# Kernel optimization log

Measured on AMD Instinct MI355X. Metric: run time of the kernel, lower is better.

Reference implementation:

```python
import jax, jax.numpy as jnp
import numpy as np

N_T = 200
THR = 0.6
ALPHA = 0.8   # hard-coded in __init__
KAPPA = 0.8   # hard-coded in __init__
RHO = 0.97
BETA = 0.07
SCALE = 50.0  # get_pos scale
# norse defaults used by ConstantCurrentLIFEncoder / LILinearCell
DT = 1e-3
TAU_MEM_INV = 100.0
TAU_SYN_INV = 200.0
V_TH = 1.0


def encode_constant_current(I):
    """norse ConstantCurrentLIFEncoder: LIF driven by constant current I [n_b, f] -> spikes [n_t, n_b, f]."""
    def step(v, _):
        v = v + DT * TAU_MEM_INV * (I - v)          # dv = dt*tau_mem_inv*((v_leak - v) + I), v_leak=0
        z = (v > V_TH).astype(I.dtype)
        v = v * (1.0 - z)                            # reset to v_reset=0 on spike
        return v, z
    _, zs = jax.lax.scan(step, jnp.zeros_like(I), None, length=N_T)
    return zs


def setup_inputs() -> dict:
    key = jax.random.key(0)
    ks = jax.random.split(key, 5)
    n_b, n_feat = 128, 512
    n_in, n_rec, n_out = 2 * n_feat, 2048, 32
    x = jax.random.normal(ks[0], (n_b, n_feat), jnp.float32)
    # kaiming_normal_ std = sqrt(2/fan_in), then scaled by w_init_gain
    w_in = jax.random.normal(ks[1], (n_rec, n_in), jnp.float32) * (0.5 * np.sqrt(2.0 / n_in))
    w_rec = jax.random.normal(ks[2], (n_rec, n_rec), jnp.float32) * (0.1 * np.sqrt(2.0 / n_rec))
    w_out = jax.random.normal(ks[3], (n_out, n_rec), jnp.float32) * (0.5 * np.sqrt(2.0 / n_rec))
    w_li = jax.random.normal(ks[4], (1, n_rec), jnp.float32) * np.sqrt(2.0 / n_rec)
    return {"x": x, "w_in": w_in, "w_rec": w_rec, "w_out": w_out, "w_li": w_li}


def reference(x, w_in, w_rec, w_out, w_li):
    n_rec = w_rec.shape[0]
    n_out = w_out.shape[0]
    n_b = x.shape[0]
    # get_pos: pos/neg rectified constant-current LIF encoding, cat on feature dim -> [n_t, n_b, n_in]
    xs = jnp.concatenate([
        encode_constant_current(jax.nn.relu(SCALE * x)),
        encode_constant_current(jax.nn.relu(-SCALE * x)),
    ], axis=2)
    # zero self-recurrence: w_rec *= (1 - I)
    w_rec = w_rec * (1.0 - jnp.eye(n_rec, dtype=w_rec.dtype))

    def step(carry, x_t):
        v, a, z, vo, li_v, li_i = carry
        # ALIF membrane update + adaptive threshold spike
        v = ALPHA * v + z @ w_rec.T + x_t @ w_in.T - z * THR
        a = RHO * a + z
        z = (v > THR + BETA * a).astype(v.dtype)
        # (dropout p=0.5 treated as identity / eval mode)
        vo = KAPPA * vo + z @ w_out.T
        # norse LILinearCell critic readout (li_step)
        i_jump = li_i + z @ w_li.T
        li_v = li_v + DT * TAU_MEM_INV * (i_jump - li_v)
        li_i = i_jump - DT * TAU_SYN_INV * i_jump
        return (v, a, z, vo, li_v, li_i), (vo, li_v)

    zeros = lambda d: jnp.zeros((n_b, d), x.dtype)
    carry0 = (zeros(n_rec), zeros(n_rec), zeros(n_rec), zeros(n_out), zeros(1), zeros(1))
    _, (vo_seq, vc_seq) = jax.lax.scan(step, carry0, xs[: N_T - 1])  # loop runs n_t-1 steps
    # torch.max over time includes the all-zero t=0 row -> clamp max with 0
    m = jnp.maximum(jnp.max(vo_seq, axis=0), 0.0)          # [n_b, n_out]
    yo = jax.nn.softmax(m, axis=1)
    critic_value = jnp.maximum(jnp.max(vc_seq, axis=0), 0.0)  # [n_b, 1]
    return yo, critic_value
```

## Files before the change

### kernel.cpp

```cpp
#include <hip/hip_runtime.h>
#include <cstdint>
#include <cstddef>

typedef __attribute__((ext_vector_type(8))) short short8;
typedef __attribute__((ext_vector_type(4))) float f32x4;
typedef __attribute__((ext_vector_type(4))) unsigned int u32x4;

union U4S8 { u32x4 u; short8 s; unsigned w[4]; };

#define TSTEPS 199

#define WF_PLANE 786432u
#define WR_BASE  1572864u
#define WR_PLANE 12288u

#define WS_BAR  0u
#define WS_ZB   4096u
#define WS_FIN  135168u
#define WS_XSB  151552u
#define WS_WF   3411968u
#define WS_NEED 28971008u

#define AT_RLX __ATOMIC_RELAXED
#define SC_AGT __HIP_MEMORY_SCOPE_AGENT

extern "C" __global__ __launch_bounds__(1024) void k_encode(
    const float* __restrict__ x, unsigned char* __restrict__ xsb)
{
  const int b = blockIdx.x;
  const int tid = threadIdx.x;
  const float xv = (tid < 512) ? x[b * 512 + tid] : x[b * 512 + tid - 512];
  const float I = (tid < 512) ? fmaxf(__fmul_rn(50.0f, xv), 0.0f)
                              : fmaxf(__fmul_rn(-50.0f, xv), 0.0f);
  float v = 0.0f;
  unsigned long long* dst =
      (unsigned long long*)(xsb + (size_t)b * 128u + (size_t)(tid >> 6) * 8u);
  for (int t = 0; t < TSTEPS; ++t) {
    v = __fadd_rn(v, __fmul_rn(0.1f, __fsub_rn(I, v)));
    const bool z = v > 1.0f;
    if (z) v = 0.0f;
    const unsigned long long m = __ballot(z ? 1 : 0);
    if ((tid & 63) == 0) dst[(size_t)t * 2048u] = m;
  }
}

__device__ __forceinline__ unsigned bf16rne(float f) {
  const unsigned u = __float_as_uint(f);
  return ((u + 0x7FFFu + ((u >> 16) & 1u)) >> 16) & 0xFFFFu;
}

extern "C" __global__ __launch_bounds__(256) void k_prep(
    const float* __restrict__ w_rec, const float* __restrict__ w_in,
    const float* __restrict__ w_out, const float* __restrict__ w_li,
    u32x4* __restrict__ wf)
{
  const unsigned idx  = blockIdx.x * 256u + threadIdx.x;
  const unsigned lane = idx & 63u;
  if (idx < 786432u) {
    const unsigned kt = (idx >> 6) % 96u;
    const unsigned ns = idx / 6144u;
    const unsigned j  = ns * 16u + (lane & 15u);
    const unsigned k0 = kt * 32u + (lane >> 4) * 8u;
    unsigned hi[4], lo[4];
#pragma unroll
    for (int u2 = 0; u2 < 4; ++u2) {
      unsigned hb[2], lb[2];
#pragma unroll
      for (int c = 0; c < 2; ++c) {
        const unsigned k = k0 + 2u * (unsigned)u2 + (unsigned)c;
        float w;
        if (k < 2048u) w = (k == j) ? 0.0f : w_rec[(size_t)j * 2048u + k];
        else           w = w_in[(size_t)j * 1024u + (k - 2048u)];
        const unsigned h = bf16rne(w);
        const float hvf = __uint_as_float(h << 16);
        const unsigned l = bf16rne(__fsub_rn(w, hvf));
        hb[c] = h; lb[c] = l;
      }
      hi[u2] = hb[0] | (hb[1] << 16);
      lo[u2] = lb[0] | (lb[1] << 16);
    }
    u32x4 vh, vl;
    vh[0]=hi[0]; vh[1]=hi[1]; vh[2]=hi[2]; vh[3]=hi[3];
    vl[0]=lo[0]; vl[1]=lo[1]; vl[2]=lo[2]; vl[3]=lo[3];
    wf[idx] = vh;
    wf[idx + WF_PLANE] = vl;
  } else if (idx < 786432u + 12288u) {
    const unsigned r   = idx - 786432u;
    const unsigned kt  = (r >> 6) & 63u;
    const unsigned nsr = r >> 12;
    const unsigned o   = nsr * 16u + (lane & 15u);
    const unsigned k0  = kt * 32u + (lane >> 4) * 8u;
    unsigned hi[4], lo[4];
#pragma unroll
    for (int u2 = 0; u2 < 4; ++u2) {
      unsigned hb[2], lb[2];
#pragma unroll
      for (int c = 0; c < 2; ++c) {
        const unsigned k = k0 + 2u * (unsigned)u2 + (unsigned)c;
        float w = 0.0f;
        if (o < 32u)       w = w_out[(size_t)o * 2048u + k];
        else if (o == 32u) w = w_li[k];
        const unsigned h = bf16rne(w);
        const float hvf = __uint_as_float(h << 16);
        hb[c] = h;
        lb[c] = bf16rne(__fsub_rn(w, hvf));
      }
      hi[u2] = hb[0] | (hb[1] << 16);
      lo[u2] = lb[0] | (lb[1] << 16);
    }
    u32x4 vh, vl;
    vh[0]=hi[0]; vh[1]=hi[1]; vh[2]=hi[2]; vh[3]=hi[3];
    vl[0]=lo[0]; vl[1]=lo[1]; vl[2]=lo[2]; vl[3]=lo[3];
    wf[WR_BASE + r] = vh;
    wf[WR_BASE + WR_PLANE + r] = vl;
  }
}

__device__ __forceinline__ void bar_arrive(unsigned* dbar, unsigned ns)
{
  __syncthreads();
  if (threadIdx.x == 0) {
    __hip_atomic_fetch_add(dbar + (ns >> 4) * 16u, 1u, AT_RLX, SC_AGT);
  }
}

__device__ __forceinline__ void bar_wait16(unsigned* dbar, unsigned tgt16)
{
  if (threadIdx.x == 0) {
    for (;;) {
      unsigned mn = 0xFFFFFFFFu;
#pragma unroll
      for (int g = 0; g < 8; ++g) {
        const unsigned c = __hip_atomic_load(dbar + g * 16, AT_RLX, SC_AGT);
        mn = (c < mn) ? c : mn;
      }
      if (mn >= tgt16) break;
      __builtin_amdgcn_s_sleep(2);
    }
    asm volatile("" ::: "memory");
  }
  __syncthreads();
}

extern "C" __global__ __launch_bounds__(512) void k_main(
    const u32x4* __restrict__ wf,
    const unsigned char* __restrict__ xsb,
    unsigned* __restrict__ zb,
    unsigned* __restrict__ bar,
    unsigned* __restrict__ fin,
    float* __restrict__ out)
{
  __shared__ unsigned abytes[64][100];
  __shared__ float red[8][64][17];
  __shared__ unsigned char zn[64][4];
  __shared__ float pad_lds[6000];

  const unsigned tid  = threadIdx.x;
  const unsigned wg   = blockIdx.x;
  const unsigned mh   = wg >> 7;
  const unsigned ns   = wg & 127u;
  const unsigned wv   = tid >> 6;
  const unsigned lane = tid & 63u;
  const unsigned ln15 = lane & 15u;
  const unsigned g4   = lane >> 4;
  const unsigned selr = g4 * 0x01010101u;
  const unsigned blq  = tid & 63u;
  const unsigned q    = tid >> 6;
  const bool     upd  = tid < 256u;
  const bool     dual = ns < 3u;

  if (tid == 0) ((volatile float*)pad_lds)[0] = 0.f;

  unsigned* dbar = bar + mh * 256u;

  const u32x4* WH = wf + (size_t)ns * 6144u;
  const u32x4* WL = wf + WF_PLANE + (size_t)ns * 6144u;
  const u32x4* RH = wf + WR_BASE + (size_t)ns * 4096u;
  const u32x4* RL = wf + WR_BASE + WR_PLANE + (size_t)ns * 4096u;

  float v[4]  = {0,0,0,0}, a[4] = {0,0,0,0}, zf[4] = {0,0,0,0};
  float vo[4] = {0,0,0,0}, voMax[4] = {0,0,0,0};
  float liv = 0.f, lii = 0.f, liMax = 0.f;

  f32x4 accX0 = {0,0,0,0}, accX1 = {0,0,0,0}, accX2 = {0,0,0,0}, accX3 = {0,0,0,0};
  U4S8 bhZ[8], blZ[8];
  const int zk = (int)wv * 8;
  const int xk = 64 + (int)wv * 4;

  auto pk = [](unsigned long long t) -> unsigned {
    return (unsigned)(t & 0xFFFFu) | (unsigned)(((t >> 32) & 0xFFFFu) << 16);
  };

  auto stage_xs = [&](int t) {
    const unsigned char* xr = xsb + ((size_t)t * 128u + mh * 64u) * 128u;
    const u32x4 val = *(const u32x4*)(xr + (size_t)lane * 128u + wv * 16u);
    *(u32x4*)&abytes[lane][64u + wv * 4u] = val;
  };

  auto mk = [&](unsigned dw, U4S8& af) {
    const unsigned sp = __builtin_amdgcn_perm(dw, dw, selr);
    const unsigned W  = ((sp >> 1) & 0xFFFF0000u) | (sp & 0x0000FFFFu);
    af.w[0] = __umul24(W & 0x00010001u, 0x3F80u);
    af.w[1] = __umul24(W & 0x00040004u, 0x0FE0u);
    af.w[2] = __umul24(W & 0x00100010u, 0x03F8u);
    af.w[3] = __umul24(W & 0x00400040u, 0x00FEu);
  };

  auto dosub2 = [&](unsigned dw, const short8& bhj, const short8& blj, f32x4& ACC) {
    U4S8 af; mk(dw, af);
    ACC = __builtin_amdgcn_mfma_f32_16x16x32_bf16(af.s, bhj, ACC, 0, 0, 0);
    ACC = __builtin_amdgcn_mfma_f32_16x16x32_bf16(af.s, blj, ACC, 0, 0, 0);
  };

  auto ldw = [&](const u32x4* H, const u32x4* L, int kb, U4S8* bh, U4S8* bl) {
#pragma unroll
    for (int j = 0; j < 4; ++j) {
      bh[j].u = H[(size_t)(kb + j) * 64u + lane];
      bl[j].u = L[(size_t)(kb + j) * 64u + lane];
    }
  };

  auto grp4 = [&](int kb, const U4S8* bh, const U4S8* bl) {
    U4S8 a0, a1, a2, a3;
    a0.u = *(const u32x4*)&abytes[ 0 + ln15][kb];
    a1.u = *(const u32x4*)&abytes[16 + ln15][kb];
    a2.u = *(const u32x4*)&abytes[32 + ln15][kb];
    a3.u = *(const u32x4*)&abytes[48 + ln15][kb];
#pragma unroll
    for (int j = 0; j < 4; ++j) {
      dosub2(a0.w[j], bh[j].s, bl[j].s, accX0);
      dosub2(a1.w[j], bh[j].s, bl[j].s, accX1);
      dosub2(a2.w[j], bh[j].s, bl[j].s, accX2);
      dosub2(a3.w[j], bh[j].s, bl[j].s, accX3);
    }
  };

  auto compute_accX = [&]() {
    U4S8 bh2[4], bl2[4];
    accX0 = {0,0,0,0}; accX1 = {0,0,0,0}; accX2 = {0,0,0,0}; accX3 = {0,0,0,0};
    ldw(WH, WL, xk, bh2, bl2);
    grp4(xk, bh2, bl2);
  };

  auto prefetchZ = [&]() {
#pragma unroll
    for (int j = 0; j < 8; ++j) {
      bhZ[j].u = WH[(size_t)(zk + j) * 64u + lane];
      blZ[j].u = WL[(size_t)(zk + j) * 64u + lane];
    }
  };

  auto stage_and_zpart = [&](unsigned buf) {
    const unsigned long long* zp = (const unsigned long long*)zb +
        ((size_t)((buf * 2u + mh) * 64u + lane) * 64u) + (unsigned)zk;
    unsigned long long z0 = __hip_atomic_load(zp + 0, AT_RLX, SC_AGT);
    unsigned long long z1 = __hip_atomic_load(zp + 1, AT_RLX, SC_AGT);
    unsigned long long z2 = __hip_atomic_load(zp + 2, AT_RLX, SC_AGT);
    unsigned long long z3 = __hip_atomic_load(zp + 3, AT_RLX, SC_AGT);
    unsigned long long z4 = __hip_atomic_load(zp + 4, AT_RLX, SC_AGT);
    unsigned long long z5 = __hip_atomic_load(zp + 5, AT_RLX, SC_AGT);
    unsigned long long z6 = __hip_atomic_load(zp + 6, AT_RLX, SC_AGT);
    unsigned long long z7 = __hip_atomic_load(zp + 7, AT_RLX, SC_AGT);
    u32x4 wa; wa[0] = pk(z0); wa[1] = pk(z1); wa[2] = pk(z2); wa[3] = pk(z3);
    *(u32x4*)&abytes[lane][(unsigned)zk] = wa;
    grp4(zk, &bhZ[0], &blZ[0]);
    u32x4 wb; wb[0] = pk(z4); wb[1] = pk(z5); wb[2] = pk(z6); wb[3] = pk(z7);
    *(u32x4*)&abytes[lane][(unsigned)zk + 4u] = wb;
    grp4(zk + 4, &bhZ[4], &blZ[4]);
  };

  auto redstore = [&]() {
#pragma unroll
    for (int r = 0; r < 4; ++r) {
      red[wv][ 0 + g4 * 4 + r][ln15] = accX0[r];
      red[wv][16 + g4 * 4 + r][ln15] = accX1[r];
      red[wv][32 + g4 * 4 + r][ln15] = accX2[r];
      red[wv][48 + g4 * 4 + r][ln15] = accX3[r];
    }
  };

  auto readout_pass = [&]() {
    f32x4 r0 = {0,0,0,0}, r1 = {0,0,0,0}, r2 = {0,0,0,0}, r3 = {0,0,0,0};
    const int kb = (int)wv * 8;
#pragma unroll
    for (int kc = 0; kc < 8; kc += 4) {
      U4S8 ar0, ar1, ar2, ar3;
      ar0.u = *(const u32x4*)&abytes[ 0 + ln15][kb + kc];
      ar1.u = *(const u32x4*)&abytes[16 + ln15][kb + kc];
      ar2.u = *(const u32x4*)&abytes[32 + ln15][kb + kc];
      ar3.u = *(const u32x4*)&abytes[48 + ln15][kb + kc];
      U4S8 bh[4], bl[4];
#pragma unroll
      for (int j = 0; j < 4; ++j) {
        bh[j].u = RH[(size_t)(kb + kc + j) * 64u + lane];
        bl[j].u = RL[(size_t)(kb + kc + j) * 64u + lane];
      }
#pragma unroll
      for (int j = 0; j < 4; ++j) {
        U4S8 af0; mk(ar0.w[j], af0);
        r0 = __builtin_amdgcn_mfma_f32_16x16x32_bf16(af0.s, bh[j].s, r0, 0, 0, 0);
        r0 = __builtin_amdgcn_mfma_f32_16x16x32_bf16(af0.s, bl[j].s, r0, 0, 0, 0);
        U4S8 af1; mk(ar1.w[j], af1);
        r1 = __builtin_amdgcn_mfma_f32_16x16x32_bf16(af1.s, bh[j].s, r1, 0, 0, 0);
        r1 = __builtin_amdgcn_mfma_f32_16x16x32_bf16(af1.s, bl[j].s, r1, 0, 0, 0);
        U4S8 af2; mk(ar2.w[j], af2);
        r2 = __builtin_amdgcn_mfma_f32_16x16x32_bf16(af2.s, bh[j].s, r2, 0, 0, 0);
        r2 = __builtin_amdgcn_mfma_f32_16x16x32_bf16(af2.s, bl[j].s, r2, 0, 0, 0);
        U4S8 af3; mk(ar3.w[j], af3);
        r3 = __builtin_amdgcn_mfma_f32_16x16x32_bf16(af3.s, bh[j].s, r3, 0, 0, 0);
        r3 = __builtin_amdgcn_mfma_f32_16x16x32_bf16(af3.s, bl[j].s, r3, 0, 0, 0);
      }
    }
#pragma unroll
    for (int r = 0; r < 4; ++r) {
      red[wv][ 0 + g4 * 4 + r][ln15] = r0[r];
      red[wv][16 + g4 * 4 + r][ln15] = r1[r];
      red[wv][32 + g4 * 4 + r][ln15] = r2[r];
      red[wv][48 + g4 * 4 + r][ln15] = r3[r];
    }
    __syncthreads();
    if (upd) {
      if (ns < 2u) {
#pragma unroll
        for (int jj = 0; jj < 4; ++jj) {
          const unsigned n = q * 4u + (unsigned)jj;
          float s = ((red[0][blq][n] + red[1][blq][n]) + (red[2][blq][n] + red[3][blq][n]))
                  + ((red[4][blq][n] + red[5][blq][n]) + (red[6][blq][n] + red[7][blq][n]));
          vo[jj] = __fadd_rn(__fmul_rn(0.8f, vo[jj]), s);
          voMax[jj] = fmaxf(voMax[jj], vo[jj]);
        }
      } else if (q == 0u) {
        float s = ((red[0][blq][0] + red[1][blq][0]) + (red[2][blq][0] + red[3][blq][0]))
                + ((red[4][blq][0] + red[5][blq][0]) + (red[6][blq][0] + red[7][blq][0]));
        const float ij = __fadd_rn(lii, s);
        liv = __fadd_rn(liv, __fmul_rn(0.1f, __fsub_rn(ij, liv)));
        lii = __fsub_rn(ij, __fmul_rn(0.2f, ij));
        liMax = fmaxf(liMax, liv);
      }
    }
    __syncthreads();
  };

  stage_xs(0);
  compute_accX();
  prefetchZ();

  for (int t = 0; t < TSTEPS; ++t) {
    if (t > 0) bar_wait16(dbar, 16u * (unsigned)t);

    stage_and_zpart((unsigned)t & 1u);
    redstore();
    __syncthreads();

    if (upd) {
      unsigned nib = 0u;
#pragma unroll
      for (int jj = 0; jj < 4; ++jj) {
        const unsigned n = q * 4u + (unsigned)jj;
        const float dv = ((red[0][blq][n] + red[1][blq][n]) + (red[2][blq][n] + red[3][blq][n]))
                       + ((red[4][blq][n] + red[5][blq][n]) + (red[6][blq][n] + red[7][blq][n]));
        const float vv = __fsub_rn(__fadd_rn(__fmul_rn(0.8f, v[jj]), dv),
                                   __fmul_rn(zf[jj], 0.6f));
        a[jj] = __fadd_rn(__fmul_rn(0.97f, a[jj]), zf[jj]);
        const float th = __fadd_rn(0.6f, __fmul_rn(0.07f, a[jj]));
        const bool znew = vv > th;
        zf[jj] = znew ? 1.0f : 0.0f;
        v[jj] = vv;
        nib |= (znew ? 1u : 0u) << jj;
      }
      zn[blq][q] = (unsigned char)nib;
    }
    __syncthreads();

    if (tid < 64u) {
      const unsigned m16 = (unsigned)zn[tid][0] | ((unsigned)zn[tid][1] << 4) |
                           ((unsigned)zn[tid][2] << 8) | ((unsigned)zn[tid][3] << 12);
      const unsigned nb = ((unsigned)t & 1u) ^ 1u;
      __hip_atomic_store(zb + ((nb * 2u + mh) * 64u + tid) * 128u + ns, m16,
                         AT_RLX, SC_AGT);
    }
    bar_arrive(dbar, ns);

    if (t < TSTEPS - 1) stage_xs(t + 1);
    if (dual && t > 0) readout_pass();
    if (t < TSTEPS - 1) {
      compute_accX();
      prefetchZ();
    }
  }

  bar_wait16(dbar, 16u * (unsigned)TSTEPS);
  if (dual) {
    const unsigned buf = (unsigned)TSTEPS & 1u;
    const unsigned long long* zp = (const unsigned long long*)zb +
        ((size_t)((buf * 2u + mh) * 64u + lane) * 64u) + (unsigned)zk;
    u32x4 wa, wb;
    wa[0] = pk(__hip_atomic_load(zp + 0, AT_RLX, SC_AGT));
    wa[1] = pk(__hip_atomic_load(zp + 1, AT_RLX, SC_AGT));
    wa[2] = pk(__hip_atomic_load(zp + 2, AT_RLX, SC_AGT));
    wa[3] = pk(__hip_atomic_load(zp + 3, AT_RLX, SC_AGT));
    wb[0] = pk(__hip_atomic_load(zp + 4, AT_RLX, SC_AGT));
    wb[1] = pk(__hip_atomic_load(zp + 5, AT_RLX, SC_AGT));
    wb[2] = pk(__hip_atomic_load(zp + 6, AT_RLX, SC_AGT));
    wb[3] = pk(__hip_atomic_load(zp + 7, AT_RLX, SC_AGT));
    *(u32x4*)&abytes[lane][(unsigned)zk] = wa;
    *(u32x4*)&abytes[lane][(unsigned)zk + 4u] = wb;
    readout_pass();
    if (ns < 2u && upd) {
#pragma unroll
      for (int jj = 0; jj < 4; ++jj) {
        __hip_atomic_store(fin + ((size_t)mh * 64u + blq) * 32u + ns * 16u + q * 4u + (unsigned)jj,
                           __float_as_uint(voMax[jj]), AT_RLX, SC_AGT);
      }
    }
    if (ns == 2u && tid < 64u) {
      out[4096u + mh * 64u + tid] = liMax;
    }
  }
  bar_arrive(dbar, ns);

  if (ns == 0u) {
    bar_wait16(dbar, 16u * ((unsigned)TSTEPS + 1u));
    if (tid < 64u) {
      const unsigned grow = mh * 64u + tid;
      float vals[32];
#pragma unroll
      for (int o = 0; o < 32; ++o)
        vals[o] = __uint_as_float(__hip_atomic_load(fin + (size_t)grow * 32u + o,
                                                    AT_RLX, SC_AGT));
      float mx = vals[0];
#pragma unroll
      for (int o = 1; o < 32; ++o) mx = fmaxf(mx, vals[o]);
      float ssum = 0.f;
#pragma unroll
      for (int o = 0; o < 32; ++o) ssum += expf(vals[o] - mx);
      const float inv = 1.0f / ssum;
#pragma unroll
      for (int o = 0; o < 32; ++o) out[(size_t)grow * 32u + o] = expf(vals[o] - mx) * inv;
    }
  }
}

extern "C" void kernel_launch(void* const* d_in, const int* in_sizes, int n_in,
                              void* d_out, int out_size, void* d_ws, size_t ws_size,
                              hipStream_t stream)
{
  (void)in_sizes; (void)n_in; (void)out_size;
  if (ws_size < (size_t)WS_NEED) return;

  const float* x     = (const float*)d_in[0];
  const float* w_in  = (const float*)d_in[1];
  const float* w_rec = (const float*)d_in[2];
  const float* w_out = (const float*)d_in[3];
  const float* w_li  = (const float*)d_in[4];
  unsigned char* ws  = (unsigned char*)d_ws;

  unsigned*      bar  = (unsigned*)(ws + WS_BAR);
  unsigned*      zb   = (unsigned*)(ws + WS_ZB);
  unsigned*      fin  = (unsigned*)(ws + WS_FIN);
  unsigned char* xsb  = ws + WS_XSB;
  u32x4*         wf   = (u32x4*)(ws + WS_WF);

  hipMemsetAsync(bar, 0, 4096, stream);
  hipMemsetAsync(zb, 0, 131072, stream);
  k_encode<<<dim3(128), dim3(1024), 0, stream>>>(x, xsb);
  k_prep<<<dim3(3120), dim3(256), 0, stream>>>(w_rec, w_in, w_out, w_li, wf);
  k_main<<<dim3(256), dim3(512), 0, stream>>>(wf, xsb, zb, bar, fin, (float*)d_out);
}
```

Baseline: 1.793 ms.

## Replace grid barrier with tagged spike ring buffer and keep weights in registers

```diff
diff --git a/kernel.cpp b/kernel.cpp
--- a/kernel.cpp
+++ b/kernel.cpp
@@ -14,12 +14,12 @@
 #define WR_BASE  1572864u
 #define WR_PLANE 12288u
 
-#define WS_BAR  0u
-#define WS_ZB   4096u
-#define WS_FIN  135168u
-#define WS_XSB  151552u
-#define WS_WF   3411968u
-#define WS_NEED 28971008u
+#define WS_BAR    0u
+#define WS_ZROLL  4096u
+#define WS_FIN    528384u
+#define WS_XSB    544768u
+#define WS_WF     3805184u
+#define WS_NEED   29364224u
 
 #define AT_RLX __ATOMIC_RELAXED
 #define SC_AGT __HIP_MEMORY_SCOPE_AGENT
@@ -116,36 +116,10 @@
   }
 }
 
-__device__ __forceinline__ void bar_arrive(unsigned* dbar, unsigned ns)
-{
-  __syncthreads();
-  if (threadIdx.x == 0) {
-    __hip_atomic_fetch_add(dbar + (ns >> 4) * 16u, 1u, AT_RLX, SC_AGT);
-  }
-}
-
-__device__ __forceinline__ void bar_wait16(unsigned* dbar, unsigned tgt16)
-{
-  if (threadIdx.x == 0) {
-    for (;;) {
-      unsigned mn = 0xFFFFFFFFu;
-#pragma unroll
-      for (int g = 0; g < 8; ++g) {
-        const unsigned c = __hip_atomic_load(dbar + g * 16, AT_RLX, SC_AGT);
-        mn = (c < mn) ? c : mn;
-      }
-      if (mn >= tgt16) break;
-      __builtin_amdgcn_s_sleep(2);
-    }
-    asm volatile("" ::: "memory");
-  }
-  __syncthreads();
-}
-
-extern "C" __global__ __launch_bounds__(512) void k_main(
+extern "C" __global__ __launch_bounds__(512, 2) void k_main(
     const u32x4* __restrict__ wf,
     const unsigned char* __restrict__ xsb,
-    unsigned* __restrict__ zb,
+    unsigned* __restrict__ zroll,
     unsigned* __restrict__ bar,
     unsigned* __restrict__ fin,
     float* __restrict__ out)
@@ -171,8 +145,6 @@
 
   if (tid == 0) ((volatile float*)pad_lds)[0] = 0.f;
 
-  unsigned* dbar = bar + mh * 256u;
-
   const u32x4* WH = wf + (size_t)ns * 6144u;
   const u32x4* WL = wf + WF_PLANE + (size_t)ns * 6144u;
   const u32x4* RH = wf + WR_BASE + (size_t)ns * 4096u;
@@ -184,17 +156,16 @@
 
   f32x4 accX0 = {0,0,0,0}, accX1 = {0,0,0,0}, accX2 = {0,0,0,0}, accX3 = {0,0,0,0};
   U4S8 bhZ[8], blZ[8];
+  U4S8 bhX[4], blX[4];
   const int zk = (int)wv * 8;
   const int xk = 64 + (int)wv * 4;
 
   auto pk = [](unsigned long long t) -> unsigned {
     return (unsigned)(t & 0xFFFFu) | (unsigned)(((t >> 32) & 0xFFFFu) << 16);
   };
-
-  auto stage_xs = [&](int t) {
-    const unsigned char* xr = xsb + ((size_t)t * 128u + mh * 64u) * 128u;
-    const u32x4 val = *(const u32x4*)(xr + (size_t)lane * 128u + wv * 16u);
-    *(u32x4*)&abytes[lane][64u + wv * 4u] = val;
+  auto tagok = [](unsigned long long z, unsigned tg) -> bool {
+    return (((unsigned)(z >> 16) & 0xFFFFu) == tg) &&
+           (((unsigned)(z >> 48) & 0xFFFFu) == tg);
   };
 
   auto mk = [&](unsigned dw, U4S8& af) {
@@ -212,14 +183,6 @@
     ACC = __builtin_amdgcn_mfma_f32_16x16x32_bf16(af.s, blj, ACC, 0, 0, 0);
   };
 
-  auto ldw = [&](const u32x4* H, const u32x4* L, int kb, U4S8* bh, U4S8* bl) {
-#pragma unroll
-    for (int j = 0; j < 4; ++j) {
-      bh[j].u = H[(size_t)(kb + j) * 64u + lane];
-      bl[j].u = L[(size_t)(kb + j) * 64u + lane];
-    }
-  };
-
   auto grp4 = [&](int kb, const U4S8* bh, const U4S8* bl) {
     U4S8 a0, a1, a2, a3;
     a0.u = *(const u32x4*)&abytes[ 0 + ln15][kb];
@@ -236,35 +199,37 @@
   };
 
   auto compute_accX = [&]() {
-    U4S8 bh2[4], bl2[4];
     accX0 = {0,0,0,0}; accX1 = {0,0,0,0}; accX2 = {0,0,0,0}; accX3 = {0,0,0,0};
-    ldw(WH, WL, xk, bh2, bl2);
-    grp4(xk, bh2, bl2);
-  };
-
-  auto prefetchZ = [&]() {
-#pragma unroll
-    for (int j = 0; j < 8; ++j) {
-      bhZ[j].u = WH[(size_t)(zk + j) * 64u + lane];
-      blZ[j].u = WL[(size_t)(zk + j) * 64u + lane];
-    }
-  };
-
-  auto stage_and_zpart = [&](unsigned buf) {
-    const unsigned long long* zp = (const unsigned long long*)zb +
-        ((size_t)((buf * 2u + mh) * 64u + lane) * 64u) + (unsigned)zk;
-    unsigned long long z0 = __hip_atomic_load(zp + 0, AT_RLX, SC_AGT);
-    unsigned long long z1 = __hip_atomic_load(zp + 1, AT_RLX, SC_AGT);
-    unsigned long long z2 = __hip_atomic_load(zp + 2, AT_RLX, SC_AGT);
-    unsigned long long z3 = __hip_atomic_load(zp + 3, AT_RLX, SC_AGT);
-    unsigned long long z4 = __hip_atomic_load(zp + 4, AT_RLX, SC_AGT);
-    unsigned long long z5 = __hip_atomic_load(zp + 5, AT_RLX, SC_AGT);
-    unsigned long long z6 = __hip_atomic_load(zp + 6, AT_RLX, SC_AGT);
-    unsigned long long z7 = __hip_atomic_load(zp + 7, AT_RLX, SC_AGT);
-    u32x4 wa; wa[0] = pk(z0); wa[1] = pk(z1); wa[2] = pk(z2); wa[3] = pk(z3);
+    grp4(xk, bhX, blX);
+  };
+
+  auto spin_load = [&](int t, unsigned long long* z) {
+    const unsigned tg = (unsigned)t & 0xFFFFu;
+    const unsigned long long* zp = (const unsigned long long*)zroll +
+        ((size_t)((((unsigned)t & 7u) * 2u + mh) * 64u + lane) * 64u) + (unsigned)zk;
+    for (;;) {
+      z[0] = __hip_atomic_load(zp + 0, AT_RLX, SC_AGT);
+      z[1] = __hip_atomic_load(zp + 1, AT_RLX, SC_AGT);
+      z[2] = __hip_atomic_load(zp + 2, AT_RLX, SC_AGT);
+      z[3] = __hip_atomic_load(zp + 3, AT_RLX, SC_AGT);
+      z[4] = __hip_atomic_load(zp + 4, AT_RLX, SC_AGT);
+      z[5] = __hip_atomic_load(zp + 5, AT_RLX, SC_AGT);
+      z[6] = __hip_atomic_load(zp + 6, AT_RLX, SC_AGT);
+      z[7] = __hip_atomic_load(zp + 7, AT_RLX, SC_AGT);
+      bool ok = tagok(z[0], tg) && tagok(z[1], tg) && tagok(z[2], tg) && tagok(z[3], tg)
+             && tagok(z[4], tg) && tagok(z[5], tg) && tagok(z[6], tg) && tagok(z[7], tg);
+      if (__all(ok ? 1 : 0)) break;
+      __builtin_amdgcn_s_sleep(2);
+    }
+  };
+
+  auto stage_and_zpart = [&](int t) {
+    unsigned long long z[8];
+    spin_load(t, z);
+    u32x4 wa; wa[0] = pk(z[0]); wa[1] = pk(z[1]); wa[2] = pk(z[2]); wa[3] = pk(z[3]);
     *(u32x4*)&abytes[lane][(unsigned)zk] = wa;
     grp4(zk, &bhZ[0], &blZ[0]);
-    u32x4 wb; wb[0] = pk(z4); wb[1] = pk(z5); wb[2] = pk(z6); wb[3] = pk(z7);
+    u32x4 wb; wb[0] = pk(z[4]); wb[1] = pk(z[5]); wb[2] = pk(z[6]); wb[3] = pk(z[7]);
     *(u32x4*)&abytes[lane][(unsigned)zk + 4u] = wb;
     grp4(zk + 4, &bhZ[4], &blZ[4]);
   };
@@ -341,14 +306,25 @@
     __syncthreads();
   };
 
-  stage_xs(0);
+#pragma unroll
+  for (int j = 0; j < 8; ++j) {
+    bhZ[j].u = WH[(size_t)(zk + j) * 64u + lane];
+    blZ[j].u = WL[(size_t)(zk + j) * 64u + lane];
+  }
+#pragma unroll
+  for (int j = 0; j < 4; ++j) {
+    bhX[j].u = WH[(size_t)(xk + j) * 64u + lane];
+    blX[j].u = WL[(size_t)(xk + j) * 64u + lane];
+  }
+  {
+    const unsigned char* xr = xsb + ((size_t)0 * 128u + mh * 64u) * 128u;
+    const u32x4 xsv = *(const u32x4*)(xr + (size_t)lane * 128u + wv * 16u);
+    *(u32x4*)&abytes[lane][64u + wv * 4u] = xsv;
+  }
   compute_accX();
-  prefetchZ();
 
   for (int t = 0; t < TSTEPS; ++t) {
-    if (t > 0) bar_wait16(dbar, 16u * (unsigned)t);
-
-    stage_and_zpart((unsigned)t & 1u);
+    stage_and_zpart(t);
     redstore();
     __syncthreads();
 
@@ -375,52 +351,54 @@
     if (tid < 64u) {
       const unsigned m16 = (unsigned)zn[tid][0] | ((unsigned)zn[tid][1] << 4) |
                            ((unsigned)zn[tid][2] << 8) | ((unsigned)zn[tid][3] << 12);
-      const unsigned nb = ((unsigned)t & 1u) ^ 1u;
-      __hip_atomic_store(zb + ((nb * 2u + mh) * 64u + tid) * 128u + ns, m16,
-                         AT_RLX, SC_AGT);
-    }
-    bar_arrive(dbar, ns);
-
-    if (t < TSTEPS - 1) stage_xs(t + 1);
-    if (dual && t > 0) readout_pass();
+      const unsigned word = m16 | (((unsigned)(t + 1) & 0xFFFFu) << 16);
+      __hip_atomic_store(zroll + ((((unsigned)(t + 1) & 7u) * 2u + mh) * 64u + tid) * 128u + ns,
+                         word, AT_RLX, SC_AGT);
+    }
+
     if (t < TSTEPS - 1) {
+      const unsigned char* xr = xsb + ((size_t)(t + 1) * 128u + mh * 64u) * 128u;
+      const u32x4 xsv = *(const u32x4*)(xr + (size_t)lane * 128u + wv * 16u);
+      if (dual && t > 0) readout_pass();
+      *(u32x4*)&abytes[lane][64u + wv * 4u] = xsv;
       compute_accX();
-      prefetchZ();
-    }
-  }
-
-  bar_wait16(dbar, 16u * (unsigned)TSTEPS);
+    } else {
+      if (dual && t > 0) readout_pass();
+    }
+  }
+
   if (dual) {
-    const unsigned buf = (unsigned)TSTEPS & 1u;
-    const unsigned long long* zp = (const unsigned long long*)zb +
-        ((size_t)((buf * 2u + mh) * 64u + lane) * 64u) + (unsigned)zk;
-    u32x4 wa, wb;
-    wa[0] = pk(__hip_atomic_load(zp + 0, AT_RLX, SC_AGT));
-    wa[1] = pk(__hip_atomic_load(zp + 1, AT_RLX, SC_AGT));
-    wa[2] = pk(__hip_atomic_load(zp + 2, AT_RLX, SC_AGT));
-    wa[3] = pk(__hip_atomic_load(zp + 3, AT_RLX, SC_AGT));
-    wb[0] = pk(__hip_atomic_load(zp + 4, AT_RLX, SC_AGT));
-    wb[1] = pk(__hip_atomic_load(zp + 5, AT_RLX, SC_AGT));
-    wb[2] = pk(__hip_atomic_load(zp + 6, AT_RLX, SC_AGT));
-    wb[3] = pk(__hip_atomic_load(zp + 7, AT_RLX, SC_AGT));
+    unsigned long long z[8];
+    spin_load(TSTEPS, z);
+    u32x4 wa; wa[0] = pk(z[0]); wa[1] = pk(z[1]); wa[2] = pk(z[2]); wa[3] = pk(z[3]);
+    u32x4 wb; wb[0] = pk(z[4]); wb[1] = pk(z[5]); wb[2] = pk(z[6]); wb[3] = pk(z[7]);
     *(u32x4*)&abytes[lane][(unsigned)zk] = wa;
     *(u32x4*)&abytes[lane][(unsigned)zk + 4u] = wb;
     readout_pass();
-    if (ns < 2u && upd) {
-#pragma unroll
-      for (int jj = 0; jj < 4; ++jj) {
-        __hip_atomic_store(fin + ((size_t)mh * 64u + blq) * 32u + ns * 16u + q * 4u + (unsigned)jj,
-                           __float_as_uint(voMax[jj]), AT_RLX, SC_AGT);
-      }
+    if (ns < 2u) {
+      if (upd) {
+#pragma unroll
+        for (int jj = 0; jj < 4; ++jj) {
+          __hip_atomic_store(fin + ((size_t)mh * 64u + blq) * 32u + ns * 16u + q * 4u + (unsigned)jj,
+                             __float_as_uint(voMax[jj]), AT_RLX, SC_AGT);
+        }
+      }
+      __syncthreads();
+      if (tid == 0) __hip_atomic_fetch_add(bar + mh * 16u, 1u, AT_RLX, SC_AGT);
     }
     if (ns == 2u && tid < 64u) {
       out[4096u + mh * 64u + tid] = liMax;
     }
   }
-  bar_arrive(dbar, ns);
 
   if (ns == 0u) {
-    bar_wait16(dbar, 16u * ((unsigned)TSTEPS + 1u));
+    if (tid == 0) {
+      while (__hip_atomic_load(bar + mh * 16u, AT_RLX, SC_AGT) < 2u) {
+        __builtin_amdgcn_s_sleep(2);
+      }
+      asm volatile("" ::: "memory");
+    }
+    __syncthreads();
     if (tid < 64u) {
       const unsigned grow = mh * 64u + tid;
       float vals[32];
@@ -455,15 +433,14 @@
   const float* w_li  = (const float*)d_in[4];
   unsigned char* ws  = (unsigned char*)d_ws;
 
-  unsigned*      bar  = (unsigned*)(ws + WS_BAR);
-  unsigned*      zb   = (unsigned*)(ws + WS_ZB);
-  unsigned*      fin  = (unsigned*)(ws + WS_FIN);
-  unsigned char* xsb  = ws + WS_XSB;
-  u32x4*         wf   = (u32x4*)(ws + WS_WF);
-
-  hipMemsetAsync(bar, 0, 4096, stream);
-  hipMemsetAsync(zb, 0, 131072, stream);
+  unsigned*      bar   = (unsigned*)(ws + WS_BAR);
+  unsigned*      zroll = (unsigned*)(ws + WS_ZROLL);
+  unsigned*      fin   = (unsigned*)(ws + WS_FIN);
+  unsigned char* xsb   = ws + WS_XSB;
+  u32x4*         wf    = (u32x4*)(ws + WS_WF);
+
+  hipMemsetAsync(ws, 0, 4096u + 524288u, stream);
   k_encode<<<dim3(128), dim3(1024), 0, stream>>>(x, xsb);
   k_prep<<<dim3(3120), dim3(256), 0, stream>>>(w_rec, w_in, w_out, w_li, wf);
-  k_main<<<dim3(256), dim3(512), 0, stream>>>(wf, xsb, zb, bar, fin, (float*)d_out);
+  k_main<<<dim3(256), dim3(512), 0, stream>>>(wf, xsb, zroll, bar, fin, (float*)d_out);
 }
```

Result: slower. 1.933 ms (+7.8%).
